# Performance work log

Hardware: AMD Instinct MI355X
Metric: run time of the kernel (lower is better)

Reference implementation:

```python
import jax, jax.numpy as jnp
import numpy as np

B, IN, CB, HD, EXP, OUT, FC1 = 512, 512, 8, 256, 128, 512, 1024
CH = CB * HD            # 2048, combiner output channels
CC = IN + CH            # 2560, concat feature size
EPS = 1e-5

def _lrelu(x):
    return jnp.where(x >= 0, x, 0.2 * x)

def _bn2(x, g, b):  # BatchNorm1d on (B, C): stats over batch
    m = x.mean(0)
    v = x.var(0)
    return (x - m) * jax.lax.rsqrt(v + EPS) * g + b

def _bn3(x, g, b):  # BatchNorm1d/2d on (B, C, L): stats over (batch, length)
    m = x.mean((0, 2), keepdims=True)
    v = x.var((0, 2), keepdims=True)
    return (x - m) * jax.lax.rsqrt(v + EPS) * g[None, :, None] + b[None, :, None]

def _cmix(W, x):  # 1x1 conv over channels: (O,I) x (B,I,L) -> (B,O,L)
    return jnp.einsum('oi,bil->bol', W, x)

def setup_inputs() -> dict:
    key = jax.random.key(0)
    ks = jax.random.split(key, 16)
    def w(k, o, i):
        return jax.random.normal(k, (o, i), jnp.float32) * (1.0 / np.sqrt(i))
    u = jax.random.uniform(ks[1], (B, CB, HD, 1), jnp.float32, 1e-6, 1.0 - 1e-6)
    return {
        'x': jax.random.normal(ks[0], (B, IN), jnp.float32),
        'gumbel': -jnp.log(-jnp.log(u)),
        # combiner (Linear no-bias + BN + LeakyReLU) x3
        'cW1': w(ks[2], 2 * IN, IN), 'cg1': jnp.ones(2 * IN), 'cb1': jnp.zeros(2 * IN),
        'cW2': w(ks[3], 2 * IN, 2 * IN), 'cg2': jnp.ones(2 * IN), 'cb2': jnp.zeros(2 * IN),
        'cW3': w(ks[4], CH, 2 * IN), 'cg3': jnp.ones(CH), 'cb3': jnp.zeros(CH),
        # encoder Conv2d1x1 stack 1 -> 32 -> 64 -> 128
        'eW1': w(ks[5], EXP // 4, 1), 'eg1': jnp.ones(EXP // 4), 'eb1': jnp.zeros(EXP // 4),
        'eW2': w(ks[6], EXP // 2, EXP // 4), 'eg2': jnp.ones(EXP // 2), 'eb2': jnp.zeros(EXP // 2),
        'eW3': w(ks[7], EXP, EXP // 2), 'eg3': jnp.ones(EXP), 'eb3': jnp.zeros(EXP),
        # fc Conv1d1x1: 2560 -> 1024 (BN+lrelu), 1024 -> OUT (bias, no act)
        'fW1': w(ks[8], FC1, CC), 'fg1': jnp.ones(FC1), 'fb1': jnp.zeros(FC1),
        'fW2': w(ks[9], OUT, FC1), 'fbias2': jnp.zeros(OUT),
        # decoder Conv1d1x1: 128 -> 64 -> 32 -> 1
        'dW1': w(ks[10], EXP // 2, EXP), 'dg1': jnp.ones(EXP // 2), 'db1': jnp.zeros(EXP // 2),
        'dW2': w(ks[11], EXP // 4, EXP // 2), 'dg2': jnp.ones(EXP // 4), 'db2': jnp.zeros(EXP // 4),
        'dW3': w(ks[12], 1, EXP // 4), 'dbias3': jnp.zeros(1),
    }

def _forward(x, gumbel, cW1, cg1, cb1, cW2, cg2, cb2, cW3, cg3, cb3,
             eW1, eg1, eb1, eW2, eg2, eb2, eW3, eg3, eb3,
             fW1, fg1, fb1, fW2, fbias2,
             dW1, dg1, db1, dW2, dg2, db2, dW3, dbias3):
    # ---- combiner: logits for gumbel-softmax hard codebook selection ----
    h = _lrelu(_bn2(x @ cW1.T, cg1, cb1))
    h = _lrelu(_bn2(h @ cW2.T, cg2, cb2))
    logits = _lrelu(_bn2(h @ cW3.T, cg3, cb3)).reshape(B, CB, HD, 1)
    y = jax.nn.softmax(logits + gumbel, axis=1)  # tau = 1 (torch default)
    hard = jax.nn.one_hot(jnp.argmax(y, axis=1), CB, axis=1, dtype=y.dtype)
    w = (hard - jax.lax.stop_gradient(y) + y)[..., 0]  # (B, CB, HD) straight-through
    # weight last dim is size-1, so broadcast-mul + sum(-1) against x collapses
    # exactly to w * sum_j x_j (same math, no (B,CB,HD,IN) intermediate).
    S = x.sum(-1)          # (B,)
    S2 = (x * x).sum(-1)   # (B,)
    xs = (w * S[:, None, None]).reshape(B, CH)
    xp = (w * S2[:, None, None]).reshape(B, CH)
    z = (xs * xs - xp) * 0.5
    feat = jnp.concatenate([x, z], axis=-1)  # (B, CC)
    # ---- encoder: Conv2d1x1 stack on (B,1,1,CC) == channel mix over length CC ----
    t = feat[:, None, :]  # (B, 1, CC)
    t = _lrelu(_bn3(_cmix(eW1, t), eg1, eb1))
    t = _lrelu(_bn3(_cmix(eW2, t), eg2, eb2))
    t = _lrelu(_bn3(_cmix(eW3, t), eg3, eb3))  # (B, EXP, CC)
    # ---- fc: Conv1d over channels=CC, length=EXP ----
    t = jnp.swapaxes(t, 1, 2)  # (B, CC, EXP)
    t = _lrelu(_bn3(_cmix(fW1, t), fg1, fb1))          # (B, FC1, EXP)
    t = _cmix(fW2, t) + fbias2[None, :, None]          # (B, OUT, EXP)
    # ---- decoder: Conv1d over channels=EXP, length=OUT ----
    t = jnp.swapaxes(t, 1, 2)  # (B, EXP, OUT)
    t = _lrelu(_bn3(_cmix(dW1, t), dg1, db1))
    t = _lrelu(_bn3(_cmix(dW2, t), dg2, db2))
    t = _cmix(dW3, t) + dbias3[None, :, None]  # (B, 1, OUT)
    return t[:, 0, :]  # (B, OUT)

def reference(x, gumbel, cW1, cg1, cb1, cW2, cg2, cb2, cW3, cg3, cb3,
              eW1, eg1, eb1, eW2, eg2, eb2, eW3, eg3, eb3,
              fW1, fg1, fb1, fW2, fbias2,
              dW1, dg1, db1, dW2, dg2, db2, dW3, dbias3):
    return _forward(x, gumbel, cW1, cg1, cb1, cW2, cg2, cb2, cW3, cg3, cb3,
                    eW1, eg1, eb1, eW2, eg2, eb2, eW3, eg3, eb3,
                    fW1, fg1, fb1, fW2, fbias2,
                    dW1, dg1, db1, dW2, dg2, db2, dW3, dbias3)
```

## Files before the change

### kernel.cpp

```cpp
#include <hip/hip_runtime.h>
#include <cstddef>

#define DEV __device__ __forceinline__
DEV float lrelu(float x){ return x >= 0.0f ? x : 0.2f*x; }
typedef _Float16 f16;
typedef _Float16 f16x8 __attribute__((ext_vector_type(8)));
typedef float f32x4 __attribute__((ext_vector_type(4)));

DEV f16x8 splat8(f16 s){ f16x8 v = {s,s,s,s,s,s,s,s}; return v; }
DEV f16x8 bnl8(f16x8 v, f16x8 sc, f16x8 sh){
    f16x8 t = v*sc + sh;
    f16x8 z = splat8((f16)0.0f);
    f16x8 mx = __builtin_elementwise_max(t, z);
    f16x8 mn = __builtin_elementwise_min(t, z);
    return mx + mn*splat8((f16)0.2f);
}

DEV void gload_lds16(const f16* src, f16* dst){
    __builtin_amdgcn_global_load_lds(
        (const __attribute__((address_space(1))) void*)src,
        (__attribute__((address_space(3))) void*)dst, 16, 0, 0);
}

DEV void dma_pair(const f16* g0, const f16* g1, f16* ldsbase, int t){
    gload_lds16(g0, ldsbase + t*8);
    gload_lds16(g1, ldsbase + 2048 + t*8);
}
DEV int swz_off(int r, int g){ return r*32 + ((g ^ ((r>>1)&3))<<3); }

#define SCHED0 __builtin_amdgcn_sched_barrier(0)
#define BARRIER __builtin_amdgcn_s_barrier()

constexpr int NXPT = 512*512;

constexpr size_t O_H1  = 0;
constexpr size_t O_H2  = O_H1 + 512*1024;
constexpr size_t O_L   = O_H2 + 512*1024;
constexpr size_t O_SEL = O_L  + 512*2048;
constexpr size_t O_S   = O_SEL + 512*256;
constexpr size_t O_S2  = O_S + 512;
constexpr size_t O_VAL = O_S2 + 512;
constexpr size_t O_PRM = O_VAL + 512;
constexpr size_t P_SC1=0, P_SH1=1024, P_SC2=2048, P_SH2=3072, P_SC3=4096, P_SH3=6144;
constexpr size_t P_A1=8192, P_C1=8224, P_EW2T=8256 ;
constexpr size_t P_ACC2=18496 , P_ACC3=18624 ;
constexpr size_t P_SCE2=18880, P_SHE2=18944, P_SCE3=19008, P_SHE3=19136;
constexpr size_t P_U0=19264 , P_FTOT=19392 ;
constexpr size_t P_SCF1=20416, P_SHF1=21440;
constexpr size_t P_SCD1=22464, P_SHD1=22528, P_SCD2=22592, P_SHD2=22624;
constexpr size_t P_SCE3H=22656, P_SHE3H=22720;
constexpr size_t P_SCF1H=22784, P_SHF1H=23296;
constexpr size_t PRM_SIZE = 32768;
constexpr size_t O_PF  = O_H1;
constexpr size_t O_PD1 = O_H2;
constexpr size_t O_PD2 = O_H2 + 8192;
constexpr size_t O_FW1H = O_L;
constexpr size_t O_FW2H = O_L + 262144;
constexpr size_t O_ACCF = O_L + 524288;
constexpr size_t O_ACCD1= O_ACCF + 2048;
constexpr size_t O_ACCD2= O_ACCD1 + 128;
constexpr size_t O_DW1H = O_L + 528384;
constexpr size_t O_EW3H = O_L + 532480;
constexpr size_t O_V2SS = O_L + 536576;
constexpr size_t O_U1  = O_PRM + PRM_SIZE;
constexpr size_t O_P1  = O_U1 + 512*128;
constexpr size_t O_FZT = O_P1 + 512*1024;
constexpr size_t O_V3S = O_FZT + (size_t)2048*1024;
constexpr size_t O_BIG1= O_V3S + 513*128;
constexpr size_t O_BIG2= O_BIG1 + (size_t)512*512*128/2;
constexpr size_t O_D1  = O_BIG2;
constexpr size_t O_D2  = O_BIG2 + (size_t)512*64*512;
constexpr size_t O_END = O_BIG2 + (size_t)512*1024*128/2;

#define FMA44(av,bv) do{ \
  acc[0][0]=fmaf(av.x,bv.x,acc[0][0]); acc[0][1]=fmaf(av.x,bv.y,acc[0][1]); \
  acc[0][2]=fmaf(av.x,bv.z,acc[0][2]); acc[0][3]=fmaf(av.x,bv.w,acc[0][3]); \
  acc[1][0]=fmaf(av.y,bv.x,acc[1][0]); acc[1][1]=fmaf(av.y,bv.y,acc[1][1]); \
  acc[1][2]=fmaf(av.y,bv.z,acc[1][2]); acc[1][3]=fmaf(av.y,bv.w,acc[1][3]); \
  acc[2][0]=fmaf(av.z,bv.x,acc[2][0]); acc[2][1]=fmaf(av.z,bv.y,acc[2][1]); \
  acc[2][2]=fmaf(av.z,bv.z,acc[2][2]); acc[2][3]=fmaf(av.z,bv.w,acc[2][3]); \
  acc[3][0]=fmaf(av.w,bv.x,acc[3][0]); acc[3][1]=fmaf(av.w,bv.y,acc[3][1]); \
  acc[3][2]=fmaf(av.w,bv.z,acc[3][2]); acc[3][3]=fmaf(av.w,bv.w,acc[3][3]); \
}while(0)

__global__ void k_sentinel(float* out){ out[blockIdx.x*256 + threadIdx.x] = 1.0e6f; }

__global__ __launch_bounds__(256) void k_prep(
    const float* __restrict__ fW1, const float* __restrict__ fW2,
    const float* __restrict__ dW1, const float* __restrict__ eW3,
    f16* __restrict__ fW1h, f16* __restrict__ fW2h, f16* __restrict__ dW1h,
    f16* __restrict__ eW3h, float* __restrict__ accAll)
{
    const int i = blockIdx.x*256 + threadIdx.x;
// ... 13 lines not shown
    const int n0 = blockIdx.x * 64, m0 = blockIdx.y * 64;
    const int t = threadIdx.x;
    const int kk = t & 15, ri = t >> 4;
    const int tx = t & 15, ty = t >> 4;
    float acc[4][4] = {{0.f,0.f,0.f,0.f},{0.f,0.f,0.f,0.f},{0.f,0.f,0.f,0.f},{0.f,0.f,0.f,0.f}};
    for (int k0 = 0; k0 < K; k0 += 16) {
        float scv = 0.f, shv = 0.f;
        if (sc) { scv = sc[k0+kk]; shv = sh[k0+kk]; }
        #pragma unroll
        for (int mm = 0; mm < 4; ++mm) {
            float v = A[(size_t)(m0 + ri + mm*16) * K + k0 + kk];
            if (sc) v = lrelu(fmaf(v, scv, shv));
            As[kk][ri + mm*16] = v;
        }
        #pragma unroll
        for (int nn = 0; nn < 4; ++nn)
            Ws[kk][ri + nn*16] = W[(size_t)(n0 + ri + nn*16) * K + k0 + kk];
        __syncthreads();
        #pragma unroll
        for (int kq = 0; kq < 16; ++kq) {
            const float4 av = *reinterpret_cast<const float4*>(&As[kq][ty*4]);
            const float4 bv = *reinterpret_cast<const float4*>(&Ws[kq][tx*4]);
            FMA44(av, bv);
        }
        __syncthreads();
    }
    #pragma unroll
    for (int i = 0; i < 4; ++i)
        #pragma unroll
        for (int j = 0; j < 4; ++j)
            C[(size_t)(m0 + ty*4 + i) * N + n0 + tx*4 + j] = acc[i][j];
}

__global__ __launch_bounds__(256) void k_stats2d(const float* __restrict__ buf, int C,
    const float* __restrict__ g, const float* __restrict__ bb,
    float* __restrict__ sc, float* __restrict__ sh)
{
    const int c = blockIdx.x, t = threadIdx.x;
    float v0 = buf[(size_t)t*C + c], v1 = buf[(size_t)(t+256)*C + c];
    __shared__ float ls[256], ls2[256];
    ls[t] = v0 + v1; ls2[t] = v0*v0 + v1*v1;
    __syncthreads();
    for (int off = 128; off; off >>= 1) { if (t < off) { ls[t]+=ls[t+off]; ls2[t]+=ls2[t+off]; } __syncthreads(); }
    if (t == 0) {
        float m = ls[0]*(1.f/512.f);
        float var = fmaxf(ls2[0]*(1.f/512.f) - m*m, 0.f);
        float r = 1.0f / sqrtf(var + 1e-5f);
        float s = g[c]*r; sc[c] = s; sh[c] = bb[c] - m*s;
    }
}

__global__ __launch_bounds__(256) void k_sel(
    const float* __restrict__ Lpre, const float* __restrict__ gumbel,
    const float* __restrict__ sc, const float* __restrict__ sh, int* __restrict__ sel)
{
    const int b = blockIdx.x, hd = threadIdx.x;
    float best = -3.0e38f; int bi = 0;
    #pragma unroll
    for (int cb = 0; cb < 8; ++cb) {
        int c = cb*256 + hd;
        float v = lrelu(fmaf(Lpre[(size_t)b*2048 + c], sc[c], sh[c])) + gumbel[(size_t)b*2048 + c];
        if (v > best) { best = v; bi = cb; }
    }
    sel[b*256 + hd] = bi;
}

__global__ __launch_bounds__(256) void k_val(const float* __restrict__ x,
    float* __restrict__ S, float* __restrict__ S2, float* __restrict__ val)
{
    const int b = blockIdx.x, t = threadIdx.x;
    float v0 = x[b*512 + t], v1 = x[b*512 + t + 256];
    __shared__ float ls[256], ls2[256];
    ls[t] = v0 + v1; ls2[t] = v0*v0 + v1*v1;
    __syncthreads();
    for (int off = 128; off; off >>= 1) { if (t < off) { ls[t]+=ls[t+off]; ls2[t]+=ls2[t+off]; } __syncthreads(); }
    if (t == 0) { float s = ls[0], s2 = ls2[0]; S[b]=s; S2[b]=s2; val[b]=0.5f*(s*s - s2); }
}

__global__ __launch_bounds__(256) void k_e1params(
    const float* __restrict__ S, const float* __restrict__ S2, const float* __restrict__ val,
    const float* __restrict__ eW1, const float* __restrict__ eg1, const float* __restrict__ eb1,
    float* __restrict__ A1, float* __restrict__ C1, float* __restrict__ accs )
// ... 170 lines not shown
    if (idx < C) {
        float m = acc[idx] * invn;
        float var = fmaxf(acc[C + idx] * invn - m*m, 0.f);
        float r = 1.0f / sqrtf(var + 1e-5f);
        float s = g[idx] * r;
        float h = bb[idx] - m*s;
        sc[idx] = s; sh[idx] = h;
        if (sch) { sch[idx] = (f16)s; shh[idx] = (f16)h; }
    }
}

__global__ void k_finalize_p(const float* __restrict__ P, int C, int nPart, float invn,
                             const float* __restrict__ g, const float* __restrict__ bb,
                             float* __restrict__ sc, float* __restrict__ sh,
                             f16* __restrict__ sch, f16* __restrict__ shh)
{
    const int idx = blockIdx.x*blockDim.x + threadIdx.x;
    if (idx < C) {
        float s = 0.f, s2 = 0.f;
        for (int p = 0; p < nPart; ++p) {
            s  += P[(size_t)p*2*C + idx];
            s2 += P[(size_t)p*2*C + C + idx];
        }
        float m = s * invn;
        float var = fmaxf(s2 * invn - m*m, 0.f);
        float r = 1.0f / sqrtf(var + 1e-5f);
        float sv = g[idx] * r;
        float h = bb[idx] - m*sv;
        sc[idx] = sv; sh[idx] = h;
        if (sch) { sch[idx] = (f16)sv; shh[idx] = (f16)h; }
    }
}

__global__ __launch_bounds__(256) void k_mfma_e3(
    const f16* __restrict__ eW3h, const f16* __restrict__ V2x,
    const float* __restrict__ sc2, const float* __restrict__ sh2,
    f16* __restrict__ V3xT)
{
    __shared__ __align__(16) f16 As[128][76];
    __shared__ __align__(16) f16 Bs[128][76];
    __shared__ float scs[64], shs[64];
    const int b = blockIdx.y, l0 = blockIdx.x * 128;
    const int t = threadIdx.x;
    const int wave = t >> 6, lane = t & 63;
    const int quad = lane >> 4, l16 = lane & 15;
    const int row = t >> 1, half = t & 1;
    if (t < 64) { scs[t] = sc2[t]; shs[t] = sh2[t]; }
    __syncthreads();
    #pragma unroll
    for (int c = 0; c < 4; ++c)
        *reinterpret_cast<f16x8*>(&As[row][half*32 + c*8]) =
            *reinterpret_cast<const f16x8*>(eW3h + row*64 + half*32 + c*8);
    const f16* src = V2x + ((size_t)(b*512 + l0 + row))*64 + half*32;
    #pragma unroll
    for (int c = 0; c < 4; ++c) {
        f16x8 v = *reinterpret_cast<const f16x8*>(src + c*8);
        f16x8 o;
        #pragma unroll
        for (int e = 0; e < 8; ++e) {
            int d = half*32 + c*8 + e;
            o[e] = (f16)lrelu(fmaf(scs[d], (float)v[e], shs[d]));
        }
        *reinterpret_cast<f16x8*>(&Bs[row][half*32 + c*8]) = o;
    }
    __syncthreads();
    f32x4 acc[2][8];
    #pragma unroll
    for (int i = 0; i < 2; ++i)
        #pragma unroll
        for (int j = 0; j < 8; ++j) acc[i][j] = (f32x4){0.f,0.f,0.f,0.f};
    f16x8 a0  = *reinterpret_cast<const f16x8*>(&As[32*wave + l16][quad*8]);
    f16x8 a0b = *reinterpret_cast<const f16x8*>(&As[32*wave + l16][32 + quad*8]);
    f16x8 a1  = *reinterpret_cast<const f16x8*>(&As[32*wave + 16 + l16][quad*8]);
    f16x8 a1b = *reinterpret_cast<const f16x8*>(&As[32*wave + 16 + l16][32 + quad*8]);
    #pragma unroll
    for (int j = 0; j < 8; ++j) {
        f16x8 bj  = *reinterpret_cast<const f16x8*>(&Bs[16*j + l16][quad*8]);
        f16x8 bjb = *reinterpret_cast<const f16x8*>(&Bs[16*j + l16][32 + quad*8]);
        acc[0][j] = __builtin_amdgcn_mfma_f32_16x16x32_f16(a0,  bj,  acc[0][j], 0, 0, 0);
        acc[0][j] = __builtin_amdgcn_mfma_f32_16x16x32_f16(a0b, bjb, acc[0][j], 0, 0, 0);
        acc[1][j] = __builtin_amdgcn_mfma_f32_16x16x32_f16(a1,  bj,  acc[1][j], 0, 0, 0);
        acc[1][j] = __builtin_amdgcn_mfma_f32_16x16x32_f16(a1b, bjb, acc[1][j], 0, 0, 0);
    }
    #pragma unroll
    for (int i = 0; i < 2; ++i) {
        #pragma unroll
        for (int r = 0; r < 4; ++r) {
            int q = 32*wave + 16*i + quad*4 + r;
            #pragma unroll
            for (int j = 0; j < 8; ++j)
                V3xT[((size_t)b*128 + q)*512 + l0 + 16*j + l16] = (f16)acc[i][j][r];
        }
    }
}

__global__ __launch_bounds__(128) void k_esupport3(
    const float* __restrict__ V2s, const float* __restrict__ sc2, const float* __restrict__ sh2,
    const float* __restrict__ eW3, float* __restrict__ V3s)
{
    const int idx = blockIdx.x, q = threadIdx.x;
    __shared__ float t2s[64];
    if (q < 64) t2s[q] = lrelu(fmaf(sc2[q], V2s[idx*64 + q], sh2[q]));
    __syncthreads();
    float s = 0.f;
    #pragma unroll
    for (int d = 0; d < 64; ++d) s = fmaf(eW3[q*64 + d], t2s[d], s);
    V3s[idx*128 + q] = s;
}

__global__ __launch_bounds__(256) void k_stats_v3scan(const f16* __restrict__ V3xT, float* __restrict__ acc3)
{
    const int q = blockIdx.x & 127, half = blockIdx.x >> 7;
    const int t = threadIdx.x, wave = t >> 6, lane = t & 63;
    float s = 0.f, s2 = 0.f;
    for (int j = half*256 + wave; j < half*256 + 256; j += 4) {
        size_t r = (size_t)q + 128*(size_t)j;
        f16x8 v = *reinterpret_cast<const f16x8*>(V3xT + r*512 + lane*8);
        #pragma unroll
        for (int e = 0; e < 8; ++e) { float f = (float)v[e]; s += f; s2 += f*f; }
    }
    #pragma unroll
    for (int off = 32; off; off >>= 1) { s += __shfl_xor(s, off); s2 += __shfl_xor(s2, off); }
    __shared__ float red[8];
    if (lane == 0) { red[wave] = s; red[4 + wave] = s2; }
    __syncthreads();
    if (t == 0) {
        atomicAdd(&acc3[q],       red[0]+red[1]+red[2]+red[3]);
        atomicAdd(&acc3[128 + q], red[4]+red[5]+red[6]+red[7]);
    }
}

__global__ void k_u(const float* __restrict__ V3s, const float* __restrict__ sc3, const float* __restrict__ sh3,
                    float* __restrict__ u1, float* __restrict__ u0)
{
    const int idx = blockIdx.x*256 + threadIdx.x;
    if (idx < 513*128) {
        int i = idx >> 7, q = idx & 127;
        float tv = lrelu(fmaf(sc3[q], V3s[idx], sh3[q]));
        if (i < 512) u1[idx] = tv; else u0[q] = tv;
    }
}

__global__ __launch_bounds__(256) void k_mfma_fw1T(
    const f16* __restrict__ fW1h, const f16* __restrict__ V3xT,
    const f16* __restrict__ sceh, const f16* __restrict__ sheh,
    const float* __restrict__ u1, const float* __restrict__ u0,
    const float* __restrict__ P1, const float* __restrict__ Ftot,
    f16* __restrict__ out6T)
{
    __shared__ __align__(16) f16 lds[24576];
    const int t = threadIdx.x;
    const int wave = t >> 6, lane = t & 63;
    const int quad = lane >> 4, l16 = lane & 15;
    const int n = blockIdx.x + (blockIdx.y << 3);
    const int b = (n & 7)*64 + (n >> 6);
    const int f0 = ((n >> 3) & 7) * 128;
    const f16* Aa = V3xT + (size_t)b*65536;
    const f16* Bb = fW1h + (size_t)f0*512;
    const int sg = (t & 3) ^ ((t >> 3) & 3);
    const size_t go0 = (size_t)(t >> 2)*512 + sg*8;
    const size_t go1 = go0 + (size_t)64*512;
    const int rA0 = 32*wave + l16, rA1 = rA0 + 16;
    const f16x8 scA0 = splat8(sceh[rA0]), shA0 = splat8(sheh[rA0]);
    const f16x8 scA1 = splat8(sceh[rA1]), shA1 = splat8(sheh[rA1]);
    const int offA0 = swz_off(rA0, quad);
    const int offA1 = swz_off(rA1, quad);
    int offB[8];
    #pragma unroll
    for (int j = 0; j < 8; ++j) offB[j] = swz_off(16*j + l16, quad);
    f32x4 acc[2][8];
    #pragma unroll
    for (int i = 0; i < 2; ++i)
        #pragma unroll
        for (int j = 0; j < 8; ++j) acc[i][j] = (f32x4){0.f,0.f,0.f,0.f};
    dma_pair(Aa + go0,      Aa + go1,      lds,               t);
    dma_pair(Bb + go0,      Bb + go1,      lds + 4096,        t);
    dma_pair(Aa + 32 + go0, Aa + 32 + go1, lds + 8192,        t);
    dma_pair(Bb + 32 + go0, Bb + 32 + go1, lds + 8192 + 4096, t);
    int m = 0;
    for (int kt = 0; kt < 16; ++kt) {
        SCHED0; BARRIER; SCHED0;
        if (kt <= 13) {
            const int mp = (m >= 1) ? m - 1 : m + 2;
            const int k0 = (kt + 2) * 32;
            dma_pair(Aa + k0 + go0, Aa + k0 + go1, lds + mp*8192,        t);
            dma_pair(Bb + k0 + go0, Bb + k0 + go1, lds + mp*8192 + 4096, t);
            asm volatile("s_waitcnt vmcnt(8)" ::: "memory");
        } else if (kt == 14) {
            asm volatile("s_waitcnt vmcnt(4)" ::: "memory");
        } else {
            asm volatile("s_waitcnt vmcnt(0)" ::: "memory");
        }
        SCHED0; BARRIER; SCHED0;
        const f16* As = lds + m*8192;
        const f16* Bs = As + 4096;
        f16x8 a0 = bnl8(*reinterpret_cast<const f16x8*>(As + offA0), scA0, shA0);
        f16x8 a1 = bnl8(*reinterpret_cast<const f16x8*>(As + offA1), scA1, shA1);
        #pragma unroll
        for (int j = 0; j < 8; ++j) {
            f16x8 bj = *reinterpret_cast<const f16x8*>(Bs + offB[j]);
            acc[0][j] = __builtin_amdgcn_mfma_f32_16x16x32_f16(a0, bj, acc[0][j], 0, 0, 0);
            acc[1][j] = __builtin_amdgcn_mfma_f32_16x16x32_f16(a1, bj, acc[1][j], 0, 0, 0);
        }
        m = (m == 2) ? 0 : m + 1;
    }
    float p1j[8], p0j[8];
    #pragma unroll
    for (int j = 0; j < 8; ++j) {
        int f = f0 + 16*j + l16;
        p1j[j] = P1[b*1024 + f];
        p0j[j] = Ftot[f] - p1j[j];
    }
    #pragma unroll
    for (int i = 0; i < 2; ++i) {
        #pragma unroll
        for (int r = 0; r < 4; ++r) {
            int q = 32*wave + 16*i + quad*4 + r;
            float u1q = u1[b*128 + q], u0q = u0[q];
            #pragma unroll
            for (int j = 0; j < 8; ++j) {
                int f = f0 + 16*j + l16;
                out6T[((size_t)b*128 + q)*1024 + f] = (f16)(acc[i][j][r] + u1q*p1j[j] + u0q*p0j[j]);
            }
        }
    }
}

__global__ __launch_bounds__(256) void k_mfma_fw2T(
    const f16* __restrict__ fW2h, const f16* __restrict__ out6T,
    const f16* __restrict__ scfh, const f16* __restrict__ shfh,
    const float* __restrict__ fbias2, f16* __restrict__ out7)
{
    __shared__ __align__(16) f16 lds[24576];
    __shared__ __align__(16) f16 scL[1024];
    __shared__ __align__(16) f16 shL[1024];
    const int t = threadIdx.x;
    const int wave = t >> 6, lane = t & 63;
    const int quad = lane >> 4, l16 = lane & 15;
    const int n = blockIdx.x + (blockIdx.y << 2);
    const int b = (n & 7)*64 + (n >> 5);
    const int o0 = ((n >> 3) & 3) * 128;
    const f16* Aa = fW2h + (size_t)o0*1024;
    const f16* Bb = out6T + (size_t)b*131072;
    const int sg = (t & 3) ^ ((t >> 3) & 3);
    const size_t go0 = (size_t)(t >> 2)*1024 + sg*8;
    const size_t go1 = go0 + (size_t)64*1024;
    const int bnO = sg*8;
    const int offA0 = swz_off(32*wave + l16, quad);
    const int offA1 = swz_off(32*wave + 16 + l16, quad);
    int offB[8];
    #pragma unroll
    for (int j = 0; j < 8; ++j) offB[j] = swz_off(16*j + l16, quad);
    f32x4 acc[2][8];
    #pragma unroll
    for (int i = 0; i < 2; ++i)
        #pragma unroll
        for (int j = 0; j < 8; ++j) acc[i][j] = (f32x4){0.f,0.f,0.f,0.f};
// ... 30 lines not shown
            *reinterpret_cast<f16x8*>(Bm + t*8)        = bnl8(v0, csc, csh);
            *reinterpret_cast<f16x8*>(Bm + 2048 + t*8) = bnl8(v1, csc, csh);
        }
        asm volatile("s_waitcnt lgkmcnt(0)" ::: "memory");
        SCHED0; BARRIER; SCHED0;
        const f16* As = lds + m*8192;
        const f16* Bs = As + 4096;
        f16x8 a0 = *reinterpret_cast<const f16x8*>(As + offA0);
        f16x8 a1 = *reinterpret_cast<const f16x8*>(As + offA1);
        #pragma unroll
        for (int j = 0; j < 8; ++j) {
            f16x8 bj = *reinterpret_cast<const f16x8*>(Bs + offB[j]);
            acc[0][j] = __builtin_amdgcn_mfma_f32_16x16x32_f16(a0, bj, acc[0][j], 0, 0, 0);
            acc[1][j] = __builtin_amdgcn_mfma_f32_16x16x32_f16(a1, bj, acc[1][j], 0, 0, 0);
        }
        m = (m == 2) ? 0 : m + 1;
    }
    #pragma unroll
    for (int i = 0; i < 2; ++i) {
        #pragma unroll
        for (int r = 0; r < 4; ++r) {
            int o = o0 + 32*wave + 16*i + quad*4 + r;
            float bias = fbias2[o];
            #pragma unroll
            for (int j = 0; j < 8; ++j) {
                int q = 16*j + l16;
                out7[((size_t)b*512 + o)*128 + q] = (f16)(acc[i][j][r] + bias);
            }
        }
    }
}

__global__ __launch_bounds__(256) void k_mfma_d1(
    const f16* __restrict__ dW1h, const f16* __restrict__ out7, float* __restrict__ d1pre)
{
    __shared__ __align__(16) f16 As[64][44];
    __shared__ __align__(16) f16 Bs[128][44];
    const int b = blockIdx.y, o0 = blockIdx.x * 128;
    const int t = threadIdx.x;
    const int wave = t >> 6, lane = t & 63;
    const int quad = lane >> 4, l16 = lane & 15;
    const int row0 = t >> 2, grp = t & 3;
    const f16* Bb = out7 + (size_t)b*65536;
    f32x4 acc[8];
    #pragma unroll
    for (int j = 0; j < 8; ++j) acc[j] = (f32x4){0.f,0.f,0.f,0.f};
    for (int k0 = 0; k0 < 128; k0 += 32) {
        *reinterpret_cast<f16x8*>(&As[row0][grp*8]) =
            *reinterpret_cast<const f16x8*>(dW1h + row0*128 + k0 + grp*8);
        #pragma unroll
        for (int p = 0; p < 2; ++p) {
            const int row = row0 + 64*p;
            *reinterpret_cast<f16x8*>(&Bs[row][grp*8]) =
                *reinterpret_cast<const f16x8*>(Bb + (size_t)(o0+row)*128 + k0 + grp*8);
        }
        __syncthreads();
        f16x8 a0 = *reinterpret_cast<const f16x8*>(&As[16*wave + l16][quad*8]);
        #pragma unroll
        for (int j = 0; j < 8; ++j) {
            f16x8 bj = *reinterpret_cast<const f16x8*>(&Bs[16*j + l16][quad*8]);
            acc[j] = __builtin_amdgcn_mfma_f32_16x16x32_f16(a0, bj, acc[j], 0, 0, 0);
        }
        __syncthreads();
    }
    #pragma unroll
    for (int r = 0; r < 4; ++r) {
        int d = 16*wave + quad*4 + r;
        #pragma unroll
        for (int j = 0; j < 8; ++j) {
            int o = o0 + 16*j + l16;
            d1pre[(size_t)b*32768 + (size_t)d*512 + o] = acc[j][r];
        }
    }
}

__global__ __launch_bounds__(256) void k_stats_rows_f16_p(
    const f16* __restrict__ buf, float* __restrict__ part)
{
    const int t = threadIdx.x;
    const int c8 = (t & 127) * 8, rl = t >> 7;
    const size_t r0 = (size_t)blockIdx.x * 256;
    float s[8] = {0,0,0,0,0,0,0,0}, s2[8] = {0,0,0,0,0,0,0,0};
    for (int rr = rl; rr < 256; rr += 2) {
        f16x8 v = *reinterpret_cast<const f16x8*>(buf + (r0 + rr)*1024 + c8);
        #pragma unroll
        for (int e = 0; e < 8; ++e) { float f = (float)v[e]; s[e] += f; s2[e] += f*f; }
    }
    __shared__ float red[128*16];
    if (rl == 1) {
        #pragma unroll
        for (int e = 0; e < 8; ++e) { red[(t&127)*16 + e] = s[e]; red[(t&127)*16 + 8 + e] = s2[e]; }
    }
    __syncthreads();
    if (rl == 0) {
        float* dst = part + (size_t)blockIdx.x * 2048;
        #pragma unroll
        for (int e = 0; e < 8; ++e) {
            dst[c8 + e]        = s[e]  + red[t*16 + e];
            dst[1024 + c8 + e] = s2[e] + red[t*16 + 8 + e];
        }
    }
}

__global__ __launch_bounds__(256) void k_stats_cols_f32_p(
    const float* __restrict__ buf, int C, float* __restrict__ part)
{
    const int t = threadIdx.x;
    const int c = blockIdx.y*8 + (t >> 5);
    const int ol = t & 31;
    const int b0 = blockIdx.x*8;
    float s = 0.f, s2 = 0.f;
    for (int bb = 0; bb < 8; ++bb) {
        const float4* p4 = reinterpret_cast<const float4*>(buf + ((size_t)(b0+bb)*C + c)*512);
        #pragma unroll
        for (int i = 0; i < 4; ++i) {
            float4 v = p4[ol + 32*i];
            s  += v.x + v.y + v.z + v.w;
            s2 += v.x*v.x + v.y*v.y + v.z*v.z + v.w*v.w;
        }
    }
    #pragma unroll
    for (int off = 16; off; off >>= 1) { s += __shfl_xor(s, off); s2 += __shfl_xor(s2, off); }
    if (ol == 0) {
        part[(size_t)blockIdx.x*2*C + c]     = s;
        part[(size_t)blockIdx.x*2*C + C + c] = s2;
    }
}

__global__ __launch_bounds__(128) void k_gemm_d2(
    const float* __restrict__ dW2, const float* __restrict__ d1pre,
    const float* __restrict__ scd, const float* __restrict__ shd, float* __restrict__ d2pre)
{
    __shared__ __align__(16) float As[16][36];
    __shared__ __align__(16) float Bs[16][68];
    const int n0 = blockIdx.x * 64, b = blockIdx.y;
    const int t = threadIdx.x;
    const int kk = t & 15, ri = t >> 4;
    const int qv = t & 63, kh = t >> 6;
    const int tx = t & 15, ty = t >> 4;
    float acc[4][4] = {{0.f,0.f,0.f,0.f},{0.f,0.f,0.f,0.f},{0.f,0.f,0.f,0.f},{0.f,0.f,0.f,0.f}};
    for (int k0 = 0; k0 < 64; k0 += 16) {
        #pragma unroll
        for (int mm = 0; mm < 4; ++mm)
            As[kk][ri + mm*8] = dW2[(ri + mm*8)*64 + k0 + kk];
        #pragma unroll
        for (int ki = 0; ki < 8; ++ki) {
            int d = k0 + kh + ki*2;
            float v = d1pre[(size_t)b*32768 + (size_t)d*512 + n0 + qv];
            Bs[kh + ki*2][qv] = lrelu(fmaf(scd[d], v, shd[d]));
        }
        __syncthreads();
        #pragma unroll
        for (int kq = 0; kq < 16; ++kq) {
            const float4 av = *reinterpret_cast<const float4*>(&As[kq][ty*4]);
            const float4 bv = *reinterpret_cast<const float4*>(&Bs[kq][tx*4]);
            FMA44(av, bv);
        }
        __syncthreads();
    }
    #pragma unroll
    for (int i = 0; i < 4; ++i)
        #pragma unroll
        for (int j = 0; j < 4; ++j)
            d2pre[(size_t)b*16384 + (size_t)(ty*4 + i)*512 + n0 + tx*4 + j] = acc[i][j];
}

__global__ __launch_bounds__(256) void k_d3(
    const float* __restrict__ d2pre, const float* __restrict__ dW3,
    const float* __restrict__ sce, const float* __restrict__ she,
    const float* __restrict__ dbias3, float* __restrict__ out)
{
    const int idx = blockIdx.x*256 + threadIdx.x;
    const int b = idx >> 9, o = idx & 511;
    float s = dbias3[0];
    for (int e = 0; e < 32; ++e) {
        float v = d2pre[(size_t)b*16384 + e*512 + o];
        s = fmaf(dW3[e], lrelu(fmaf(v, sce[e], she[e])), s);
    }
    out[idx] = s;
}

// ... 34 lines not shown
    const float* dg2 = (const float*)d_in[29];
    const float* db2 = (const float*)d_in[30];
    const float* dW3 = (const float*)d_in[31];
    const float* dbias3 = (const float*)d_in[32];
    float* out = (float*)d_out;
    float* ws  = (float*)d_ws;

    if (ws_size < O_END * sizeof(float)) {
        k_sentinel<<<1024,256,0,stream>>>(out);
        return;
    }

    float* H1  = ws + O_H1;
    float* H2  = ws + O_H2;
    float* L   = ws + O_L;
    int*   sel = (int*)(ws + O_SEL);
    float* S   = ws + O_S;
    float* S2  = ws + O_S2;
    float* val = ws + O_VAL;
    float* prm = ws + O_PRM;
    f16*   fW1h= (f16*)(ws + O_FW1H);
    f16*   fW2h= (f16*)(ws + O_FW2H);
    float* accF= ws + O_ACCF;
    f16*   dW1h= (f16*)(ws + O_DW1H);
    f16*   eW3h= (f16*)(ws + O_EW3H);
    float* V2s = ws + O_V2SS;
    float* u1  = ws + O_U1;
    float* P1  = ws + O_P1;
    float* fzT = ws + O_FZT;
    float* V3s = ws + O_V3S;
    float* pF  = ws + O_PF;
    float* pD1 = ws + O_PD1;
    float* pD2 = ws + O_PD2;
    f16*   V3xT= (f16*)(ws + O_BIG1);
    f16*   out7= (f16*)(ws + O_BIG1);
    f16*   out6T=(f16*)(ws + O_BIG2);
    f16*   V2x = (f16*)(ws + O_BIG2);
    float* d1p = ws + O_D1;
    float* d2p = ws + O_D2;

    const float invN_e = 1.0f/1310720.f;

    k_gemm_c<<<dim3(16,8),256,0,stream>>>(x,  cW1, H1, 1024, 512,  nullptr,     nullptr);
    k_stats2d<<<1024,256,0,stream>>>(H1, 1024, cg1, cb1, prm+P_SC1, prm+P_SH1);
    k_gemm_c<<<dim3(16,8),256,0,stream>>>(H1, cW2, H2, 1024, 1024, prm+P_SC1, prm+P_SH1);
    k_stats2d<<<1024,256,0,stream>>>(H2, 1024, cg2, cb2, prm+P_SC2, prm+P_SH2);
    k_gemm_c<<<dim3(32,8),256,0,stream>>>(H2, cW3, L,  2048, 1024, prm+P_SC2, prm+P_SH2);
    k_stats2d<<<2048,256,0,stream>>>(L, 2048, cg3, cb3, prm+P_SC3, prm+P_SH3);
    k_sel<<<512,256,0,stream>>>(L, gumbel, prm+P_SC3, prm+P_SH3, sel);

    k_prep<<<2048,256,0,stream>>>(fW1, fW2, dW1, eW3, fW1h, fW2h, dW1h, eW3h, accF);
    k_val<<<512,256,0,stream>>>(x, S, S2, val);
    k_e1params<<<1,256,0,stream>>>(S, S2, val, eW1, eg1, eb1, prm+P_A1, prm+P_C1, prm+P_ACC2);
    k_transpose_fz<<<dim3(32,16),256,0,stream>>>(fW1, fzT);
    k_wtrans2<<<1,256,0,stream>>>(eW2, prm+P_EW2T);
    k_ftot<<<4,256,0,stream>>>(fzT, prm+P_FTOT);
    k_p1<<<512,256,0,stream>>>(fzT, sel, P1);

    k_epass2<<<1024,256,0,stream>>>(x, prm+P_A1, prm+P_C1, prm+P_EW2T, V2x);
    k_esupport2<<<513,64,0,stream>>>(val, prm+P_A1, prm+P_C1, prm+P_EW2T, V2s);
    k_stats_v2scan<<<64,256,0,stream>>>(V2x, prm+P_ACC2);
    k_wstats<<<64,64,0,stream>>>(V2s, 64, prm+P_ACC2);
    k_finalize<<<1,256,0,stream>>>(prm+P_ACC2, 64, invN_e, eg2, eb2, prm+P_SCE2, prm+P_SHE2,
                                   nullptr, nullptr);
    k_mfma_e3<<<dim3(4,512),256,0,stream>>>(eW3h, V2x, prm+P_SCE2, prm+P_SHE2, V3xT);
    k_esupport3<<<513,128,0,stream>>>(V2s, prm+P_SCE2, prm+P_SHE2, eW3, V3s);
    k_stats_v3scan<<<256,256,0,stream>>>(V3xT, prm+P_ACC3);
    k_wstats<<<128,64,0,stream>>>(V3s, 128, prm+P_ACC3);
    k_finalize<<<1,256,0,stream>>>(prm+P_ACC3, 128, invN_e, eg3, eb3, prm+P_SCE3, prm+P_SHE3,
                                   (f16*)(prm+P_SCE3H), (f16*)(prm+P_SHE3H));
    k_u<<<257,256,0,stream>>>(V3s, prm+P_SCE3, prm+P_SHE3, u1, prm+P_U0);

    k_mfma_fw1T<<<dim3(8,512),256,0,stream>>>(fW1h, V3xT,
                                              (const f16*)(prm+P_SCE3H), (const f16*)(prm+P_SHE3H),
                                              u1, prm+P_U0, P1, prm+P_FTOT, out6T);
    k_stats_rows_f16_p<<<256,256,0,stream>>>(out6T, pF);
    k_finalize_p<<<4,256,0,stream>>>(pF, 1024, 256, 1.0f/65536.f, fg1, fb1,
                                     prm+P_SCF1, prm+P_SHF1,
                                     (f16*)(prm+P_SCF1H), (f16*)(prm+P_SHF1H));
    k_mfma_fw2T<<<dim3(4,512),256,0,stream>>>(fW2h, out6T,
                                              (const f16*)(prm+P_SCF1H), (const f16*)(prm+P_SHF1H),
                                              fbias2, out7);

    k_mfma_d1<<<dim3(4,512),256,0,stream>>>(dW1h, out7, d1p);
    k_stats_cols_f32_p<<<dim3(64,8),256,0,stream>>>(d1p, 64, pD1);
    k_finalize_p<<<1,64,0,stream>>>(pD1, 64, 64, 1.0f/262144.f, dg1, db1,
                                    prm+P_SCD1, prm+P_SHD1, nullptr, nullptr);
    k_gemm_d2<<<dim3(8,512),128,0,stream>>>(dW2, d1p, prm+P_SCD1, prm+P_SHD1, d2p);
    k_stats_cols_f32_p<<<dim3(64,4),256,0,stream>>>(d2p, 32, pD2);
    k_finalize_p<<<1,32,0,stream>>>(pD2, 32, 64, 1.0f/262144.f, dg2, db2,
                                    prm+P_SCD2, prm+P_SHD2, nullptr, nullptr);
    k_d3<<<1024,256,0,stream>>>(d2p, dW3, prm+P_SCD2, prm+P_SHD2, dbias3, out);
}
```

Before: 985.2 us.

## Fuse BatchNorm statistics into GEMM epilogues and store d1 activations in fp16

The separate statistics scans over V3xT, out6T and d1pre are removed. Instead the MFMA kernels (e3, fw1T, d1) compute per-block partial sums and sums of squares in their epilogues and write them to partial buffers, which new finalize kernels reduce. The per-channel combiner stats kernel is replaced by a coalesced float4 partial-sum kernel plus finalize, and d1pre is now stored as fp16, halving its traffic. The gain is fewer full passes over large intermediates. The cost is extra shuffles, LDS reductions and barriers in the GEMM epilogues, serial single-block finalize loops, and reduced precision on d1.

```diff
diff --git a/kernel.cpp b/kernel.cpp
--- a/kernel.cpp
+++ b/kernel.cpp
@@ -53,12 +53,10 @@
 constexpr size_t PRM_SIZE = 32768;
 constexpr size_t O_PF  = O_H1;
 constexpr size_t O_PD1 = O_H2;
-constexpr size_t O_PD2 = O_H2 + 8192;
+constexpr size_t O_PD2 = O_H2 + 262144;
 constexpr size_t O_FW1H = O_L;
 constexpr size_t O_FW2H = O_L + 262144;
 constexpr size_t O_ACCF = O_L + 524288;
-constexpr size_t O_ACCD1= O_ACCF + 2048;
-constexpr size_t O_ACCD2= O_ACCD1 + 128;
 constexpr size_t O_DW1H = O_L + 528384;
 constexpr size_t O_EW3H = O_L + 532480;
 constexpr size_t O_V2SS = O_L + 536576;
@@ -138,22 +136,21 @@
             C[(size_t)(m0 + ty*4 + i) * N + n0 + tx*4 + j] = acc[i][j];
 }
 
-__global__ __launch_bounds__(256) void k_stats2d(const float* __restrict__ buf, int C,
-    const float* __restrict__ g, const float* __restrict__ bb,
-    float* __restrict__ sc, float* __restrict__ sh)
-{
-    const int c = blockIdx.x, t = threadIdx.x;
-    float v0 = buf[(size_t)t*C + c], v1 = buf[(size_t)(t+256)*C + c];
-    __shared__ float ls[256], ls2[256];
-    ls[t] = v0 + v1; ls2[t] = v0*v0 + v1*v1;
-    __syncthreads();
-    for (int off = 128; off; off >>= 1) { if (t < off) { ls[t]+=ls[t+off]; ls2[t]+=ls2[t+off]; } __syncthreads(); }
-    if (t == 0) {
-        float m = ls[0]*(1.f/512.f);
-        float var = fmaxf(ls2[0]*(1.f/512.f) - m*m, 0.f);
-        float r = 1.0f / sqrtf(var + 1e-5f);
-        float s = g[c]*r; sc[c] = s; sh[c] = bb[c] - m*s;
-    }
+__global__ __launch_bounds__(256) void k_stats2d_p(
+    const float* __restrict__ buf, int C, float* __restrict__ part)
+{
+    const int t = threadIdx.x;
+    const int r0 = blockIdx.x*16;
+    const int c0 = blockIdx.y*1024;
+    float s[4]={0.f,0.f,0.f,0.f}, s2[4]={0.f,0.f,0.f,0.f};
+    for (int rr = 0; rr < 16; ++rr) {
+        float4 v = *reinterpret_cast<const float4*>(buf + (size_t)(r0+rr)*C + c0 + t*4);
+        s[0]+=v.x; s[1]+=v.y; s[2]+=v.z; s[3]+=v.w;
+        s2[0]+=v.x*v.x; s2[1]+=v.y*v.y; s2[2]+=v.z*v.z; s2[3]+=v.w*v.w;
+    }
+    float* d0 = part + (size_t)blockIdx.x*2*C + c0 + t*4;
+    *reinterpret_cast<float4*>(d0)     = (float4){s[0],s[1],s[2],s[3]};
+    *reinterpret_cast<float4*>(d0 + C) = (float4){s2[0],s2[1],s2[2],s2[3]};
 }
 
 __global__ __launch_bounds__(256) void k_sel(
@@ -390,14 +387,88 @@
     }
 }
 
+__global__ __launch_bounds__(256) void k_finalize_e3(
+    const float* __restrict__ P, const float* __restrict__ accw,
+    const float* __restrict__ g, const float* __restrict__ bb,
+    float* __restrict__ sc, float* __restrict__ sh,
+    f16* __restrict__ sch, f16* __restrict__ shh)
+{
+    const int t = threadIdx.x, q = t & 127, h = t >> 7;
+    float s = 0.f, s2 = 0.f;
+    for (int p = h*1024; p < h*1024 + 1024; ++p) {
+        s  += P[(size_t)p*256 + q];
+        s2 += P[(size_t)p*256 + 128 + q];
+    }
+    __shared__ float red[2][2][128];
+    red[h][0][q] = s; red[h][1][q] = s2;
+    __syncthreads();
+    if (t < 128) {
+        float ss  = red[0][0][q] + red[1][0][q] + accw[q];
+        float ss2 = red[0][1][q] + red[1][1][q] + accw[128 + q];
+        const float invn = 1.0f/1310720.f;
+        float m = ss * invn;
+        float var = fmaxf(ss2 * invn - m*m, 0.f);
+        float r = 1.0f / sqrtf(var + 1e-5f);
+        float sv = g[q] * r, hh = bb[q] - m*sv;
+        sc[q] = sv; sh[q] = hh; sch[q] = (f16)sv; shh[q] = (f16)hh;
+    }
+}
+
+__global__ __launch_bounds__(256) void k_finalize_f(
+    const float* __restrict__ P,
+    const float* __restrict__ g, const float* __restrict__ bb,
+    float* __restrict__ sc, float* __restrict__ sh,
+    f16* __restrict__ sch, f16* __restrict__ shh)
+{
+    const int f = blockIdx.x*256 + threadIdx.x;
+    const int fb = f >> 7, c = f & 127;
+    const float* base = P + (size_t)fb*512*256 + c;
+    float s = 0.f, s2 = 0.f;
+    for (int b = 0; b < 512; ++b) {
+        s  += base[(size_t)b*256];
+        s2 += base[(size_t)b*256 + 128];
+    }
+    float m = s*(1.0f/65536.f);
+    float var = fmaxf(s2*(1.0f/65536.f) - m*m, 0.f);
+    float r = 1.0f/sqrtf(var + 1e-5f);
+    float sv = g[f]*r, h = bb[f] - m*sv;
+    sc[f] = sv; sh[f] = h; sch[f] = (f16)sv; shh[f] = (f16)h;
+}
+
+__global__ __launch_bounds__(256) void k_finalize_d1(
+    const float* __restrict__ P,
+    const float* __restrict__ g, const float* __restrict__ bb,
+    float* __restrict__ sc, float* __restrict__ sh)
+{
+    const int t = threadIdx.x, d = t & 63, gr = t >> 6;
+    float s = 0.f, s2 = 0.f;
+    for (int p = gr*512; p < gr*512 + 512; ++p) {
+        s  += P[(size_t)p*128 + d];
+        s2 += P[(size_t)p*128 + 64 + d];
+    }
+    __shared__ float red[4][2][64];
+    red[gr][0][d] = s; red[gr][1][d] = s2;
+    __syncthreads();
+    if (t < 64) {
+        float ss  = red[0][0][t]+red[1][0][t]+red[2][0][t]+red[3][0][t];
+        float ss2 = red[0][1][t]+red[1][1][t]+red[2][1][t]+red[3][1][t];
+        float m = ss*(1.0f/262144.f);
+        float var = fmaxf(ss2*(1.0f/262144.f) - m*m, 0.f);
+        float r = 1.0f/sqrtf(var + 1e-5f);
+        float sv = g[t]*r;
+        sc[t] = sv; sh[t] = bb[t] - m*sv;
+    }
+}
+
 __global__ __launch_bounds__(256) void k_mfma_e3(
     const f16* __restrict__ eW3h, const f16* __restrict__ V2x,
     const float* __restrict__ sc2, const float* __restrict__ sh2,
-    f16* __restrict__ V3xT)
+    f16* __restrict__ V3xT, float* __restrict__ pE3)
 {
     __shared__ __align__(16) f16 As[128][76];
     __shared__ __align__(16) f16 Bs[128][76];
     __shared__ float scs[64], shs[64];
+    __shared__ float rede[256];
     const int b = blockIdx.y, l0 = blockIdx.x * 128;
     const int t = threadIdx.x;
     const int wave = t >> 6, lane = t & 63;
@@ -440,16 +511,53 @@
         acc[1][j] = __builtin_amdgcn_mfma_f32_16x16x32_f16(a1,  bj,  acc[1][j], 0, 0, 0);
         acc[1][j] = __builtin_amdgcn_mfma_f32_16x16x32_f16(a1b, bjb, acc[1][j], 0, 0, 0);
     }
+    float se[8] = {0,0,0,0,0,0,0,0}, s2e[8] = {0,0,0,0,0,0,0,0};
     #pragma unroll
     for (int i = 0; i < 2; ++i) {
         #pragma unroll
         for (int r = 0; r < 4; ++r) {
             int q = 32*wave + 16*i + quad*4 + r;
             #pragma unroll
-            for (int j = 0; j < 8; ++j)
-                V3xT[((size_t)b*128 + q)*512 + l0 + 16*j + l16] = (f16)acc[i][j][r];
-        }
-    }
+            for (int j = 0; j < 8; ++j) {
+                float v = acc[i][j][r];
+                V3xT[((size_t)b*128 + q)*512 + l0 + 16*j + l16] = (f16)v;
+                se[i*4+r] += v; s2e[i*4+r] += v*v;
+            }
+        }
+    }
+    #pragma unroll
+    for (int k = 0; k < 8; ++k) {
+        se[k]  += __shfl_xor(se[k],1);  se[k]  += __shfl_xor(se[k],2);
+        se[k]  += __shfl_xor(se[k],4);  se[k]  += __shfl_xor(se[k],8);
+        s2e[k] += __shfl_xor(s2e[k],1); s2e[k] += __shfl_xor(s2e[k],2);
+        s2e[k] += __shfl_xor(s2e[k],4); s2e[k] += __shfl_xor(s2e[k],8);
+    }
+    if (l16 == 0) {
+        #pragma unroll
+        for (int i = 0; i < 2; ++i)
+            #pragma unroll
+            for (int r = 0; r < 4; ++r) {
+                int qq = 32*wave + 16*i + quad*4 + r;
+                rede[qq] = se[i*4+r];
+            }
+    }
+    __syncthreads();
+    if (l16 == 0) {
+    }
+    float outv = rede[t & 127];
+    if (t < 128) pE3[((size_t)(blockIdx.x*512 + b))*256 + t] = outv;
+    __syncthreads();
+    if (l16 == 0) {
+        #pragma unroll
+        for (int i = 0; i < 2; ++i)
+            #pragma unroll
+            for (int r = 0; r < 4; ++r) {
+                int qq = 32*wave + 16*i + quad*4 + r;
+                rede[qq] = s2e[i*4+r];
+            }
+    }
+    __syncthreads();
+    if (t < 128) pE3[((size_t)(blockIdx.x*512 + b))*256 + 128 + t] = rede[t];
 }
 
 __global__ __launch_bounds__(128) void k_esupport3(
@@ -464,28 +572,6 @@
     #pragma unroll
     for (int d = 0; d < 64; ++d) s = fmaf(eW3[q*64 + d], t2s[d], s);
     V3s[idx*128 + q] = s;
-}
-
-__global__ __launch_bounds__(256) void k_stats_v3scan(const f16* __restrict__ V3xT, float* __restrict__ acc3)
-{
-    const int q = blockIdx.x & 127, half = blockIdx.x >> 7;
-    const int t = threadIdx.x, wave = t >> 6, lane = t & 63;
-    float s = 0.f, s2 = 0.f;
-    for (int j = half*256 + wave; j < half*256 + 256; j += 4) {
-        size_t r = (size_t)q + 128*(size_t)j;
-        f16x8 v = *reinterpret_cast<const f16x8*>(V3xT + r*512 + lane*8);
-        #pragma unroll
-        for (int e = 0; e < 8; ++e) { float f = (float)v[e]; s += f; s2 += f*f; }
-    }
-    #pragma unroll
-    for (int off = 32; off; off >>= 1) { s += __shfl_xor(s, off); s2 += __shfl_xor(s2, off); }
-    __shared__ float red[8];
-    if (lane == 0) { red[wave] = s; red[4 + wave] = s2; }
-    __syncthreads();
-    if (t == 0) {
-        atomicAdd(&acc3[q],       red[0]+red[1]+red[2]+red[3]);
-        atomicAdd(&acc3[128 + q], red[4]+red[5]+red[6]+red[7]);
-    }
 }
 
 __global__ void k_u(const float* __restrict__ V3s, const float* __restrict__ sc3, const float* __restrict__ sh3,
@@ -504,15 +590,17 @@
     const f16* __restrict__ sceh, const f16* __restrict__ sheh,
     const float* __restrict__ u1, const float* __restrict__ u0,
     const float* __restrict__ P1, const float* __restrict__ Ftot,
-    f16* __restrict__ out6T)
+    f16* __restrict__ out6T, float* __restrict__ pF)
 {
     __shared__ __align__(16) f16 lds[24576];
+    __shared__ float redf[1024];
     const int t = threadIdx.x;
     const int wave = t >> 6, lane = t & 63;
     const int quad = lane >> 4, l16 = lane & 15;
     const int n = blockIdx.x + (blockIdx.y << 3);
     const int b = (n & 7)*64 + (n >> 6);
-    const int f0 = ((n >> 3) & 7) * 128;
+    const int fblk = (n >> 3) & 7;
+    const int f0 = fblk * 128;
     const f16* Aa = V3xT + (size_t)b*65536;
     const f16* Bb = fW1h + (size_t)f0*512;
     const int sg = (t & 3) ^ ((t >> 3) & 3);
@@ -569,6 +657,9 @@
         p1j[j] = P1[b*1024 + f];
         p0j[j] = Ftot[f] - p1j[j];
     }
+    float sj[8], s2j[8];
+    #pragma unroll
+    for (int j = 0; j < 8; ++j) { sj[j] = 0.f; s2j[j] = 0.f; }
     #pragma unroll
     for (int i = 0; i < 2; ++i) {
         #pragma unroll
@@ -578,9 +669,28 @@
             #pragma unroll
             for (int j = 0; j < 8; ++j) {
                 int f = f0 + 16*j + l16;
-                out6T[((size_t)b*128 + q)*1024 + f] = (f16)(acc[i][j][r] + u1q*p1j[j] + u0q*p0j[j]);
+                float v = acc[i][j][r] + u1q*p1j[j] + u0q*p0j[j];
+                out6T[((size_t)b*128 + q)*1024 + f] = (f16)v;
+                sj[j] += v; s2j[j] += v*v;
             }
         }
+    }
+    #pragma unroll
+    for (int j = 0; j < 8; ++j) {
+        sj[j]  += __shfl_xor(sj[j],16);  sj[j]  += __shfl_xor(sj[j],32);
+        s2j[j] += __shfl_xor(s2j[j],16); s2j[j] += __shfl_xor(s2j[j],32);
+    }
+    if (quad == 0) {
+        #pragma unroll
+        for (int j = 0; j < 8; ++j) {
+            redf[wave*256 + j*16 + l16]       = sj[j];
+            redf[wave*256 + 128 + j*16 + l16] = s2j[j];
+        }
+    }
+    __syncthreads();
+    {
+        float v = redf[t] + redf[256 + t] + redf[512 + t] + redf[768 + t];
+        pF[((size_t)(fblk*512 + b))*256 + t] = v;
     }
 }
 
@@ -677,10 +787,12 @@
 }
 
 __global__ __launch_bounds__(256) void k_mfma_d1(
-    const f16* __restrict__ dW1h, const f16* __restrict__ out7, float* __restrict__ d1pre)
+    const f16* __restrict__ dW1h, const f16* __restrict__ out7,
+    f16* __restrict__ d1pre, float* __restrict__ pD1)
 {
     __shared__ __align__(16) f16 As[64][44];
     __shared__ __align__(16) f16 Bs[128][44];
+    __shared__ float redd[128];
     const int b = blockIdx.y, o0 = blockIdx.x * 128;
     const int t = threadIdx.x;
     const int wave = t >> 6, lane = t & 63;
@@ -708,43 +820,34 @@
         }
         __syncthreads();
     }
+    float sd[4] = {0,0,0,0}, s2d[4] = {0,0,0,0};
     #pragma unroll
     for (int r = 0; r < 4; ++r) {
         int d = 16*wave + quad*4 + r;
         #pragma unroll
         for (int j = 0; j < 8; ++j) {
             int o = o0 + 16*j + l16;
-            d1pre[(size_t)b*32768 + (size_t)d*512 + o] = acc[j][r];
-        }
-    }
-}
-
-__global__ __launch_bounds__(256) void k_stats_rows_f16_p(
-    const f16* __restrict__ buf, float* __restrict__ part)
-{
-    const int t = threadIdx.x;
-    const int c8 = (t & 127) * 8, rl = t >> 7;
-    const size_t r0 = (size_t)blockIdx.x * 256;
-    float s[8] = {0,0,0,0,0,0,0,0}, s2[8] = {0,0,0,0,0,0,0,0};
-    for (int rr = rl; rr < 256; rr += 2) {
-        f16x8 v = *reinterpret_cast<const f16x8*>(buf + (r0 + rr)*1024 + c8);
-        #pragma unroll
-        for (int e = 0; e < 8; ++e) { float f = (float)v[e]; s[e] += f; s2[e] += f*f; }
-    }
-    __shared__ float red[128*16];
-    if (rl == 1) {
-        #pragma unroll
-        for (int e = 0; e < 8; ++e) { red[(t&127)*16 + e] = s[e]; red[(t&127)*16 + 8 + e] = s2[e]; }
-    }
-    __syncthreads();
-    if (rl == 0) {
-        float* dst = part + (size_t)blockIdx.x * 2048;
-        #pragma unroll
-        for (int e = 0; e < 8; ++e) {
-            dst[c8 + e]        = s[e]  + red[t*16 + e];
-            dst[1024 + c8 + e] = s2[e] + red[t*16 + 8 + e];
-        }
-    }
+            float v = acc[j][r];
+            d1pre[(size_t)b*32768 + (size_t)d*512 + o] = (f16)v;
+            sd[r] += v; s2d[r] += v*v;
+        }
+    }
+    #pragma unroll
+    for (int r = 0; r < 4; ++r) {
+        sd[r]  += __shfl_xor(sd[r],1);  sd[r]  += __shfl_xor(sd[r],2);
+        sd[r]  += __shfl_xor(sd[r],4);  sd[r]  += __shfl_xor(sd[r],8);
+        s2d[r] += __shfl_xor(s2d[r],1); s2d[r] += __shfl_xor(s2d[r],2);
+        s2d[r] += __shfl_xor(s2d[r],4); s2d[r] += __shfl_xor(s2d[r],8);
+    }
+    if (l16 == 0) {
+        #pragma unroll
+        for (int r = 0; r < 4; ++r) {
+            int dd = 16*wave + quad*4 + r;
+            redd[dd] = sd[r]; redd[64 + dd] = s2d[r];
+        }
+    }
+    __syncthreads();
+    if (t < 128) pD1[((size_t)(blockIdx.x*512 + b))*128 + t] = redd[t];
 }
 
 __global__ __launch_bounds__(256) void k_stats_cols_f32_p(
@@ -773,7 +876,7 @@
 }
 
 __global__ __launch_bounds__(128) void k_gemm_d2(
-    const float* __restrict__ dW2, const float* __restrict__ d1pre,
+    const float* __restrict__ dW2, const f16* __restrict__ d1pre,
     const float* __restrict__ scd, const float* __restrict__ shd, float* __restrict__ d2pre)
 {
     __shared__ __align__(16) float As[16][36];
@@ -791,7 +894,7 @@
         #pragma unroll
         for (int ki = 0; ki < 8; ++ki) {
             int d = k0 + kh + ki*2;
-            float v = d1pre[(size_t)b*32768 + (size_t)d*512 + n0 + qv];
+            float v = (float)d1pre[(size_t)b*32768 + (size_t)d*512 + n0 + qv];
             Bs[kh + ki*2][qv] = lrelu(fmaf(scd[d], v, shd[d]));
         }
         __syncthreads();
@@ -892,21 +995,29 @@
     float* pF  = ws + O_PF;
     float* pD1 = ws + O_PD1;
     float* pD2 = ws + O_PD2;
+    float* p2d = ws + O_P1;
+    float* pE3 = ws + O_FZT;
     f16*   V3xT= (f16*)(ws + O_BIG1);
     f16*   out7= (f16*)(ws + O_BIG1);
     f16*   out6T=(f16*)(ws + O_BIG2);
     f16*   V2x = (f16*)(ws + O_BIG2);
-    float* d1p = ws + O_D1;
+    f16*   d1p = (f16*)(ws + O_D1);
     float* d2p = ws + O_D2;
 
     const float invN_e = 1.0f/1310720.f;
 
     k_gemm_c<<<dim3(16,8),256,0,stream>>>(x,  cW1, H1, 1024, 512,  nullptr,     nullptr);
-    k_stats2d<<<1024,256,0,stream>>>(H1, 1024, cg1, cb1, prm+P_SC1, prm+P_SH1);
+    k_stats2d_p<<<dim3(32,1),256,0,stream>>>(H1, 1024, p2d);
+    k_finalize_p<<<4,256,0,stream>>>(p2d, 1024, 32, 1.0f/512.f, cg1, cb1,
+                                     prm+P_SC1, prm+P_SH1, nullptr, nullptr);
     k_gemm_c<<<dim3(16,8),256,0,stream>>>(H1, cW2, H2, 1024, 1024, prm+P_SC1, prm+P_SH1);
-    k_stats2d<<<1024,256,0,stream>>>(H2, 1024, cg2, cb2, prm+P_SC2, prm+P_SH2);
+    k_stats2d_p<<<dim3(32,1),256,0,stream>>>(H2, 1024, p2d);
+    k_finalize_p<<<4,256,0,stream>>>(p2d, 1024, 32, 1.0f/512.f, cg2, cb2,
+                                     prm+P_SC2, prm+P_SH2, nullptr, nullptr);
     k_gemm_c<<<dim3(32,8),256,0,stream>>>(H2, cW3, L,  2048, 1024, prm+P_SC2, prm+P_SH2);
-    k_stats2d<<<2048,256,0,stream>>>(L, 2048, cg3, cb3, prm+P_SC3, prm+P_SH3);
+    k_stats2d_p<<<dim3(32,2),256,0,stream>>>(L, 2048, p2d);
+    k_finalize_p<<<8,256,0,stream>>>(p2d, 2048, 32, 1.0f/512.f, cg3, cb3,
+                                     prm+P_SC3, prm+P_SH3, nullptr, nullptr);
     k_sel<<<512,256,0,stream>>>(L, gumbel, prm+P_SC3, prm+P_SH3, sel);
 
     k_prep<<<2048,256,0,stream>>>(fW1, fW2, dW1, eW3, fW1h, fW2h, dW1h, eW3h, accF);
@@ -923,29 +1034,24 @@
     k_wstats<<<64,64,0,stream>>>(V2s, 64, prm+P_ACC2);
     k_finalize<<<1,256,0,stream>>>(prm+P_ACC2, 64, invN_e, eg2, eb2, prm+P_SCE2, prm+P_SHE2,
                                    nullptr, nullptr);
-    k_mfma_e3<<<dim3(4,512),256,0,stream>>>(eW3h, V2x, prm+P_SCE2, prm+P_SHE2, V3xT);
+    k_mfma_e3<<<dim3(4,512),256,0,stream>>>(eW3h, V2x, prm+P_SCE2, prm+P_SHE2, V3xT, pE3);
     k_esupport3<<<513,128,0,stream>>>(V2s, prm+P_SCE2, prm+P_SHE2, eW3, V3s);
-    k_stats_v3scan<<<256,256,0,stream>>>(V3xT, prm+P_ACC3);
     k_wstats<<<128,64,0,stream>>>(V3s, 128, prm+P_ACC3);
-    k_finalize<<<1,256,0,stream>>>(prm+P_ACC3, 128, invN_e, eg3, eb3, prm+P_SCE3, prm+P_SHE3,
-                                   (f16*)(prm+P_SCE3H), (f16*)(prm+P_SHE3H));
+    k_finalize_e3<<<1,256,0,stream>>>(pE3, prm+P_ACC3, eg3, eb3, prm+P_SCE3, prm+P_SHE3,
+                                      (f16*)(prm+P_SCE3H), (f16*)(prm+P_SHE3H));
     k_u<<<257,256,0,stream>>>(V3s, prm+P_SCE3, prm+P_SHE3, u1, prm+P_U0);
 
     k_mfma_fw1T<<<dim3(8,512),256,0,stream>>>(fW1h, V3xT,
                                               (const f16*)(prm+P_SCE3H), (const f16*)(prm+P_SHE3H),
-                                              u1, prm+P_U0, P1, prm+P_FTOT, out6T);
-    k_stats_rows_f16_p<<<256,256,0,stream>>>(out6T, pF);
-    k_finalize_p<<<4,256,0,stream>>>(pF, 1024, 256, 1.0f/65536.f, fg1, fb1,
-                                     prm+P_SCF1, prm+P_SHF1,
+                                              u1, prm+P_U0, P1, prm+P_FTOT, out6T, pF);
+    k_finalize_f<<<4,256,0,stream>>>(pF, fg1, fb1, prm+P_SCF1, prm+P_SHF1,
                                      (f16*)(prm+P_SCF1H), (f16*)(prm+P_SHF1H));
     k_mfma_fw2T<<<dim3(4,512),256,0,stream>>>(fW2h, out6T,
                                               (const f16*)(prm+P_SCF1H), (const f16*)(prm+P_SHF1H),
                                               fbias2, out7);
 
-    k_mfma_d1<<<dim3(4,512),256,0,stream>>>(dW1h, out7, d1p);
-    k_stats_cols_f32_p<<<dim3(64,8),256,0,stream>>>(d1p, 64, pD1);
-    k_finalize_p<<<1,64,0,stream>>>(pD1, 64, 64, 1.0f/262144.f, dg1, db1,
-                                    prm+P_SCD1, prm+P_SHD1, nullptr, nullptr);
+    k_mfma_d1<<<dim3(4,512),256,0,stream>>>(dW1h, out7, d1p, pD1);
+    k_finalize_d1<<<1,256,0,stream>>>(pD1, dg1, db1, prm+P_SCD1, prm+P_SHD1);
     k_gemm_d2<<<dim3(8,512),128,0,stream>>>(dW2, d1p, prm+P_SCD1, prm+P_SHD1, d2p);
     k_stats_cols_f32_p<<<dim3(64,4),256,0,stream>>>(d2p, 32, pD2);
     k_finalize_p<<<1,32,0,stream>>>(pD2, 32, 64, 1.0f/262144.f, dg2, db2,
```

Measured after the change: 935.6 us. 1.05x faster.
